# Optimization experiments

Hardware: AMD Instinct MI355X
Metric: run time of the kernel (lower is better)

## Reference

```python
import jax, jax.numpy as jnp
import numpy as np
from jax import lax

ALPHA = 0.95
THETA = 1.0
GAMMA = 12.0
GAIN = 1.0  # gain buffer value used in forward (detached in torch via .item())
KERNELS = (8, 16, 32)
B, T = 256, 16384


@jax.custom_vjp
def surrogate_spike(x):
    # forward: hard threshold at 0
    return (x >= 0).astype(x.dtype)


def _spike_fwd(x):
    return surrogate_spike(x), x


def _spike_bwd(x, g):
    ax = jnp.abs(GAMMA * x)
    grad = (ax < 1.0).astype(x.dtype) * (1.0 - ax) * GAMMA
    return (g * grad,)


surrogate_spike.defvjp(_spike_fwd, _spike_bwd)


def causal_conv(x, w):
    # x: [B,1,T], w: [1,1,k] -> [B,T]; left-pad k-1 (causal), cross-correlation like torch Conv1d
    k = w.shape[-1]
    out = lax.conv_general_dilated(
        x, w, window_strides=(1,), padding=[(k - 1, 0)],
        dimension_numbers=("NCH", "OIH", "NCH"))
    return out[:, 0, :]


def lif_wta(u):
    # u: [B,K,T] -> spikes s_all [B,K,T]
    Bb, K, Tt = u.shape

    def step(v, u_t):  # v,u_t: [B,K]
        v = ALPHA * v + u_t
        m = v - THETA
        s_raw = surrogate_spike(m)
        mask = jax.nn.one_hot(jnp.argmax(m, axis=1), K, dtype=m.dtype)  # top-1 WTA
        s = s_raw * mask
        return v - s * THETA, s

    v0 = jnp.zeros((Bb, K), u.dtype)
    _, s_all = lax.scan(step, v0, jnp.moveaxis(u, 2, 0))  # [T,B,K]
    return jnp.moveaxis(s_all, 0, 2)  # [B,K,T]


def setup_inputs() -> dict:
    key = jax.random.key(0)
    kx, k0, k1, k2, ky = jax.random.split(key, 5)
    x = jax.random.normal(kx, (B, 1, T), dtype=jnp.float32)
    w0 = jax.random.normal(k0, (1, 1, 8), dtype=jnp.float32) / np.sqrt(8.0)
    w1 = jax.random.normal(k1, (1, 1, 16), dtype=jnp.float32) / np.sqrt(16.0)
    w2 = jax.random.normal(k2, (1, 1, 32), dtype=jnp.float32) / np.sqrt(32.0)
    y = jax.random.randint(ky, (B, T), 0, 2, dtype=jnp.int32)
    return {"x": x, "w0": w0, "w1": w1, "w2": w2, "y": y}


def reference(x, w0, w1, w2, y):
    ws = (w0, w1, w2)
    # per-branch causal conv, scaled by 1/sqrt(k), then gain
    u = jnp.stack(
        [causal_conv(x, w) * (1.0 / np.sqrt(float(k))) for w, k in zip(ws, KERNELS)],
        axis=1) * GAIN  # [B,K,T]
    s_all = lif_wta(u)
    return (u, s_all)
```

## Files before the change

kernel.cpp:

```cpp
#include <hip/hip_runtime.h>
#include <math.h>

constexpr int B = 256;
constexpr int T = 16384;
constexpr int K = 3;

constexpr int CHUNK = 256;
constexpr int WARM  = 512;

constexpr int CBT = 128;
constexpr int CWT = 32;


__global__ __launch_bounds__(256, 2) void conv_kernel(
    const float* __restrict__ x,
    const float* __restrict__ w0f,
    const float* __restrict__ w1f,
    const float* __restrict__ w2f,
    float*  __restrict__ u_out,
    float*  __restrict__ w32)
{
    const int blk = blockIdx.x;
    const int bgi = blk >> 7;
    const int t0  = (blk & 127) * CBT;
    const int b0  = bgi * 64;
    const int tid = threadIdx.x;

    __shared__ float sx[64][164];
    for (int k = tid; k < 64 * 40; k += 256) {
        const int r  = k / 40;
        const int c4 = k - r * 40;
        const int g  = t0 - 32 + 4 * c4;
        float4 v = make_float4(0.f, 0.f, 0.f, 0.f);
        if (g >= 0) v = *(const float4*)(x + (size_t)(b0 + r) * T + g);
        *(float4*)&sx[r][4 * c4] = v;
    }
    __syncthreads();

    const int lane    = tid & 63;
    const int w       = tid >> 6;
    const int t_start = t0 + CWT * w;

    double w0d[8], w1d[16], w2d[32];
#pragma unroll
    for (int i = 0; i < 8; ++i)  w0d[i] = (double)w0f[i];
#pragma unroll
    for (int i = 0; i < 16; ++i) w1d[i] = (double)w1f[i];
#pragma unroll
    for (int i = 0; i < 32; ++i) w2d[i] = (double)w2f[i];

    double win[32];
#pragma unroll
    for (int k = 1; k < 32; ++k) win[k] = (double)sx[lane][CWT * w + k];

    const double s8  = 1.0 / sqrt(8.0);
    const double s32 = 1.0 / sqrt(32.0);

    float fr0[16], fr1[16], fr2[16];
    float4 pf;
    float* uf = u_out + (size_t)(b0 + lane) * (3 * T);

#define PPUT(v, D) do {                                                       \
    const float _pv = (v);                                                    \
    if (((D) & 3) == 0) pf.x = _pv;                                           \
    else if (((D) & 3) == 1) pf.y = _pv;                                      \
    else if (((D) & 3) == 2) pf.z = _pv;                                      \
    else {                                                                    \
        pf.w = _pv;                                                           \
        *(float4*)(wq + ((D) >> 2) * 256) = pf;                               \
    }                                                                         \
} while (0)

#pragma unroll
    for (int j = 0; j < CWT; ++j) {
        win[j & 31] = (double)sx[lane][CWT * w + 32 + j];
        double a0 = 0.0, a1 = 0.0, a2 = 0.0;
#pragma unroll
        for (int i = 0; i < 8; ++i)  a0 = fma(w0d[i], win[(j + 25 + i) & 31], a0);
#pragma unroll
        for (int i = 0; i < 16; ++i) a1 = fma(w1d[i], win[(j + 17 + i) & 31], a1);
#pragma unroll
        for (int i = 0; i < 32; ++i) a2 = fma(w2d[i], win[(j + 1 + i) & 31], a2);
        a0 *= s8; a1 *= 0.25; a2 *= s32;

        const int t = t_start + j;
        float* wq = w32 + ((size_t)(t >> 4) * 4 + bgi) * 3072 + lane * 4;
        const int D0 = (j & 15) * 3;
        PPUT((float)(a0 - 0.05), D0);
        PPUT((float)(a1 - 0.05), D0 + 1);
        PPUT((float)(a2 - 0.05), D0 + 2);

        fr0[j & 15] = (float)a0; fr1[j & 15] = (float)a1; fr2[j & 15] = (float)a2;
        if ((j & 15) == 15) {
            float* d = uf + t_start + (j & ~15);
#pragma unroll
            for (int q = 0; q < 4; ++q) {
                *(float4*)(d + 4 * q)         = ((float4*)fr0)[q];
                *(float4*)(d + T + 4 * q)     = ((float4*)fr1)[q];
                *(float4*)(d + 2 * T + 4 * q) = ((float4*)fr2)[q];
            }
        }
    }
#undef PPUT
}

__global__ __launch_bounds__(64, 1) void scan_kernel(
    const float* __restrict__ w32,
    float* __restrict__ s_out)
{
    const int phys = blockIdx.x;
    const int xcd  = phys & 7;
    const int slot = phys >> 3;
    const int c    = 8 * xcd + (slot & 7);
    const int bg   = slot >> 3;
    const int lane = threadIdx.x;

    const int t_emit = c * CHUNK;
    const int t_w    = (t_emit >= WARM) ? (t_emit - WARM) : 0;
    const int warm_g = (t_emit - t_w) >> 4;
    const int n_g    = warm_g + (CHUNK >> 4);
    const int tw16   = t_w >> 4;

    __shared__ float4 lbuf[3 * 768];
    __shared__ float4 sstage[12 * 65];

    double m0 = -1.0, m1 = -1.0, m2 = -1.0;

#define WAITN(N) do {                                                   \
    asm volatile("s_waitcnt vmcnt(" #N ")" ::: "memory");               \
    __builtin_amdgcn_sched_barrier(0);                                  \
} while (0)

#define LOADDMA(s, gg) do {                                                   \
    const float4* _src = (const float4*)(w32 +                                \
        ((size_t)(tw16 + (gg)) * 4 + bg) * 3072) + lane;                      \
    _Pragma("unroll")                                                         \
    for (int _q = 0; _q < 12; ++_q)                                           \
        __builtin_amdgcn_global_load_lds(                                     \
            (const __attribute__((address_space(1))) void*)(const void*)      \
                (_src + (size_t)_q * 64),                                     \
            (__attribute__((address_space(3))) void*)(void*)                  \
                (&lbuf[(s) * 768 + _q * 64]),                                 \
            16, 0, 0);                                                        \
} while (0)

#define STEP(W0, W1, W2, O0, O1, O2) do {                               \
    const double M0 = fma(0.95, m0, (W0));                              \
    const double M1 = fma(0.95, m1, (W1));                              \
    const double M2 = fma(0.95, m2, (W2));                              \
    const bool c01 = (M0 >= M1);                                        \
    const bool c02 = (M0 >= M2);                                        \
    const bool c12 = (M1 >= M2);                                        \
    const bool f0  = (M0 >= 0.0);                                       \
    const bool f1  = (M1 >= 0.0);                                       \
    const bool f2  = (M2 >= 0.0);                                       \
    const bool s0 = c01 & c02 & f0;             \
    const bool s1 = (!c01) & c12 & f1;                                  \
    const bool s2 = (!c02) & (!c12) & f2;                               \
    m0 = s0 ? M0 - 1.0 : M0;                                            \
    m1 = s1 ? M1 - 1.0 : M1;                                            \
    m2 = s2 ? M2 - 1.0 : M2;                                            \
    (O0) = s0 ? 1.0f : 0.0f;                                            \
    (O1) = s1 ? 1.0f : 0.0f;                                            \
    (O2) = s2 ? 1.0f : 0.0f;                                            \
} while (0)

#define GETW(d) ( ((d) & 3) == 0 ? _rf[(d) >> 2].x                      \
                : ((d) & 3) == 1 ? _rf[(d) >> 2].y                      \
                : ((d) & 3) == 2 ? _rf[(d) >> 2].z                      \
                :                  _rf[(d) >> 2].w )

#define BODY(s, pp) do {                                                      \
    if ((pp) < n_g) {                                                         \
        if ((pp) == n_g - 1)            WAITN(24);                            \
        else if ((pp) == n_g - 2)       WAITN(36);                            \
        else if ((pp) >= warm_g + 2)    WAITN(48);                            \
        else if ((pp) == warm_g + 1)    WAITN(36);                            \
        else                            WAITN(24);                            \
        const float4* _lp = lbuf + (s) * 768 + lane;                          \
        float4 _rf[12];                                                       \
        _Pragma("unroll")                                                     \
        for (int _q = 0; _q < 12; ++_q) _rf[_q] = _lp[(size_t)_q * 64];       \
        float sp0[16], sp1[16], sp2[16];                                      \
        _Pragma("unroll")                                                     \
        for (int _j = 0; _j < 16; ++_j) {                                     \
            const int _d0 = 3 * _j;                                           \
            const double _W0 = (double)GETW(_d0);                             \
            const double _W1 = (double)GETW(_d0 + 1);                         \
            const double _W2 = (double)GETW(_d0 + 2);                         \
            STEP(_W0, _W1, _W2, sp0[_j], sp1[_j], sp2[_j]);                   \
        }                                                                     \
        if ((pp) + 3 < n_g) LOADDMA(s, (pp) + 3);                             \
        if ((pp) >= warm_g) {                                                 \
              \
            _Pragma("unroll")                                                 \
            for (int _q = 0; _q < 4; ++_q) {                                  \
                sstage[(0 * 4 + _q) * 65 + lane] = ((float4*)sp0)[_q];        \
                sstage[(1 * 4 + _q) * 65 + lane] = ((float4*)sp1)[_q];        \
                sstage[(2 * 4 + _q) * 65 + lane] = ((float4*)sp2)[_q];        \
            }                                                                 \
            asm volatile("s_waitcnt lgkmcnt(0)" ::: "memory");                \
            __builtin_amdgcn_sched_barrier(0);                                \
              \
              \
            const int _t = t_w + (pp) * 16;                                   \
            _Pragma("unroll")                                                 \
            for (int _k = 0; _k < 3; ++_k) {                                  \
                _Pragma("unroll")                                             \
                for (int _g = 0; _g < 4; ++_g) {                              \
                    const float4 _v =                                         \
                        sstage[(_k * 4 + (lane & 3)) * 65 + _g * 16 + (lane >> 2)]; \
                    float* _dst = s_out                                       \
                        + (size_t)(bg * 64 + _g * 16 + (lane >> 2)) * (3 * T) \
                        + (size_t)_k * T + _t + (lane & 3) * 4;               \
                    *(float4*)_dst = _v;                                      \
                }                                                             \
            }                                                                 \
        }                                                                     \
    }                                                                         \
} while (0)

    LOADDMA(0, 0);
    LOADDMA(1, 1);
    LOADDMA(2, 2);
    for (int p = 0; p < n_g; p += 3) {
        BODY(0, p);
        BODY(1, p + 1);
        BODY(2, p + 2);
    }

#undef BODY
#undef GETW
#undef STEP
#undef LOADDMA
#undef WAITN
}

extern "C" void kernel_launch(void* const* d_in, const int* in_sizes, int n_in,
                              void* d_out, int out_size, void* d_ws, size_t ws_size,
                              hipStream_t stream)
{
    const float* x  = (const float*)d_in[0];
    const float* w0 = (const float*)d_in[1];
    const float* w1 = (const float*)d_in[2];
    const float* w2 = (const float*)d_in[3];

    float* out   = (float*)d_out;
    float* u_out = out;
    float* s_out = out + (size_t)B * K * T;

    float* w32 = (float*)d_ws;

    conv_kernel<<<(B / 64) * (T / CBT), 256, 0, stream>>>(x, w0, w1, w2, u_out, w32);
    scan_kernel<<<B, 64, 0, stream>>>(w32, s_out);
}
```

Before: 217.0 us.

## Split scan chunk across four waves with shared LDS ring and staggered warm-up

The scan kernel moves from one 64-lane wave per block to four waves. Each wave handles a quarter of the 256-step emit chunk and runs its own warm-up window, so the serial dependent chain each wave walks gets shorter. The waves share one 6-slot LDS ring filled by global_load_lds, with each wave issuing a third of each group's loads, and block-wide syncthreads around every group. The cost is duplicated warm-up computation, two barriers per group, and more LDS use.

```diff
diff --git a/kernel.cpp b/kernel.cpp
--- a/kernel.cpp
+++ b/kernel.cpp
@@ -104,7 +104,7 @@
 #undef PPUT
 }
 
-__global__ __launch_bounds__(64, 1) void scan_kernel(
+__global__ __launch_bounds__(256, 1) void scan_kernel(
     const float* __restrict__ w32,
     float* __restrict__ s_out)
 {
@@ -113,16 +113,20 @@
     const int slot = phys >> 3;
     const int c    = 8 * xcd + (slot & 7);
     const int bg   = slot >> 3;
-    const int lane = threadIdx.x;
+    const int tid  = threadIdx.x;
+    const int lane = tid & 63;
+    const int w    = tid >> 6;
 
     const int t_emit = c * CHUNK;
     const int t_w    = (t_emit >= WARM) ? (t_emit - WARM) : 0;
-    const int warm_g = (t_emit - t_w) >> 4;
-    const int n_g    = warm_g + (CHUNK >> 4);
     const int tw16   = t_w >> 4;
-
-    __shared__ float4 lbuf[3 * 768];
-    __shared__ float4 sstage[12 * 65];
+    const int n_g    = (t_emit >> 4) + 16 - tw16;
+    const int es     = n_g - 16 + 4 * w;
+    const int as     = (es >= 32) ? (es - 32) : 0;
+
+    __shared__ float4 ring[6 * 768];
+    __shared__ float4 sstage[4][12 * 65];
+    float4* ss = sstage[w];
 
     double m0 = -1.0, m1 = -1.0, m2 = -1.0;
 
@@ -131,16 +135,16 @@
     __builtin_amdgcn_sched_barrier(0);                                  \
 } while (0)
 
-#define LOADDMA(s, gg) do {                                                   \
+#define ISSUE(sl, gg) do {                                                    \
     const float4* _src = (const float4*)(w32 +                                \
-        ((size_t)(tw16 + (gg)) * 4 + bg) * 3072) + lane;                      \
+        ((size_t)(tw16 + (gg)) * 4 + bg) * 3072) + (size_t)(3 * w) * 64 + lane; \
     _Pragma("unroll")                                                         \
-    for (int _q = 0; _q < 12; ++_q)                                           \
+    for (int _q = 0; _q < 3; ++_q)                                            \
         __builtin_amdgcn_global_load_lds(                                     \
             (const __attribute__((address_space(1))) void*)(const void*)      \
                 (_src + (size_t)_q * 64),                                     \
             (__attribute__((address_space(3))) void*)(void*)                  \
-                (&lbuf[(s) * 768 + _q * 64]),                                 \
+                (&ring[(sl) * 768 + (3 * w + _q) * 64]),                      \
             16, 0, 0);                                                        \
 } while (0)
 
@@ -165,74 +169,75 @@
     (O2) = s2 ? 1.0f : 0.0f;                                            \
 } while (0)
 
-#define GETW(d) ( ((d) & 3) == 0 ? _rf[(d) >> 2].x                      \
-                : ((d) & 3) == 1 ? _rf[(d) >> 2].y                      \
-                : ((d) & 3) == 2 ? _rf[(d) >> 2].z                      \
-                :                  _rf[(d) >> 2].w )
-
-#define BODY(s, pp) do {                                                      \
-    if ((pp) < n_g) {                                                         \
-        if ((pp) == n_g - 1)            WAITN(24);                            \
-        else if ((pp) == n_g - 2)       WAITN(36);                            \
-        else if ((pp) >= warm_g + 2)    WAITN(48);                            \
-        else if ((pp) == warm_g + 1)    WAITN(36);                            \
-        else                            WAITN(24);                            \
-        const float4* _lp = lbuf + (s) * 768 + lane;                          \
-        float4 _rf[12];                                                       \
-        _Pragma("unroll")                                                     \
-        for (int _q = 0; _q < 12; ++_q) _rf[_q] = _lp[(size_t)_q * 64];       \
-        float sp0[16], sp1[16], sp2[16];                                      \
-        _Pragma("unroll")                                                     \
-        for (int _j = 0; _j < 16; ++_j) {                                     \
-            const int _d0 = 3 * _j;                                           \
-            const double _W0 = (double)GETW(_d0);                             \
-            const double _W1 = (double)GETW(_d0 + 1);                         \
-            const double _W2 = (double)GETW(_d0 + 2);                         \
-            STEP(_W0, _W1, _W2, sp0[_j], sp1[_j], sp2[_j]);                   \
-        }                                                                     \
-        if ((pp) + 3 < n_g) LOADDMA(s, (pp) + 3);                             \
-        if ((pp) >= warm_g) {                                                 \
-              \
-            _Pragma("unroll")                                                 \
-            for (int _q = 0; _q < 4; ++_q) {                                  \
-                sstage[(0 * 4 + _q) * 65 + lane] = ((float4*)sp0)[_q];        \
-                sstage[(1 * 4 + _q) * 65 + lane] = ((float4*)sp1)[_q];        \
-                sstage[(2 * 4 + _q) * 65 + lane] = ((float4*)sp2)[_q];        \
-            }                                                                 \
-            asm volatile("s_waitcnt lgkmcnt(0)" ::: "memory");                \
-            __builtin_amdgcn_sched_barrier(0);                                \
-              \
-              \
-            const int _t = t_w + (pp) * 16;                                   \
-            _Pragma("unroll")                                                 \
-            for (int _k = 0; _k < 3; ++_k) {                                  \
-                _Pragma("unroll")                                             \
-                for (int _g = 0; _g < 4; ++_g) {                              \
-                    const float4 _v =                                         \
-                        sstage[(_k * 4 + (lane & 3)) * 65 + _g * 16 + (lane >> 2)]; \
-                    float* _dst = s_out                                       \
-                        + (size_t)(bg * 64 + _g * 16 + (lane >> 2)) * (3 * T) \
-                        + (size_t)_k * T + _t + (lane & 3) * 4;               \
-                    *(float4*)_dst = _v;                                      \
-                }                                                             \
-            }                                                                 \
-        }                                                                     \
-    }                                                                         \
-} while (0)
-
-    LOADDMA(0, 0);
-    LOADDMA(1, 1);
-    LOADDMA(2, 2);
-    for (int p = 0; p < n_g; p += 3) {
-        BODY(0, p);
-        BODY(1, p + 1);
-        BODY(2, p + 2);
+#define GETW(d) ( ((d) & 3) == 0 ? (double)_rf[(d) >> 2].x              \
+                : ((d) & 3) == 1 ? (double)_rf[(d) >> 2].y              \
+                : ((d) & 3) == 2 ? (double)_rf[(d) >> 2].z              \
+                :                  (double)_rf[(d) >> 2].w )
+
+#pragma unroll
+    for (int g = 0; g < 6; ++g) ISSUE(g, g);
+
+    for (int p = 0; p < 48; ++p) {
+        if (p >= n_g) break;
+
+        {
+            const int d = n_g - p;
+            if (d >= 6)      WAITN(15);
+            else if (d == 5) WAITN(12);
+            else if (d == 4) WAITN(9);
+            else if (d == 3) WAITN(6);
+            else if (d == 2) WAITN(3);
+            else             WAITN(0);
+        }
+        __syncthreads();
+
+        const int sl = p % 6;
+        const bool act = (p >= as) && (p < es + 4);
+        float sp0[16], sp1[16], sp2[16];
+        if (act) {
+            const float4* _lp = ring + sl * 768 + lane;
+            float4 _rf[12];
+#pragma unroll
+            for (int _q = 0; _q < 12; ++_q) _rf[_q] = _lp[(size_t)_q * 64];
+#pragma unroll
+            for (int _j = 0; _j < 16; ++_j) {
+                const int _d0 = 3 * _j;
+                STEP(GETW(_d0), GETW(_d0 + 1), GETW(_d0 + 2),
+                     sp0[_j], sp1[_j], sp2[_j]);
+            }
+        }
+        __syncthreads();
+
+        if (p + 6 < n_g) ISSUE(sl, p + 6);
+
+        if (act && p >= es) {
+#pragma unroll
+            for (int _q = 0; _q < 4; ++_q) {
+                ss[(0 * 4 + _q) * 65 + lane] = ((float4*)sp0)[_q];
+                ss[(1 * 4 + _q) * 65 + lane] = ((float4*)sp1)[_q];
+                ss[(2 * 4 + _q) * 65 + lane] = ((float4*)sp2)[_q];
+            }
+            asm volatile("s_waitcnt lgkmcnt(0)" ::: "memory");
+            __builtin_amdgcn_sched_barrier(0);
+            const int _t = (tw16 + p) * 16;
+#pragma unroll
+            for (int _k = 0; _k < 3; ++_k) {
+#pragma unroll
+                for (int _g = 0; _g < 4; ++_g) {
+                    const float4 _v =
+                        ss[(_k * 4 + (lane & 3)) * 65 + _g * 16 + (lane >> 2)];
+                    float* _dst = s_out
+                        + (size_t)(bg * 64 + _g * 16 + (lane >> 2)) * (3 * T)
+                        + (size_t)_k * T + _t + (lane & 3) * 4;
+                    *(float4*)_dst = _v;
+                }
+            }
+        }
     }
 
-#undef BODY
 #undef GETW
 #undef STEP
-#undef LOADDMA
+#undef ISSUE
 #undef WAITN
 }
 
@@ -252,5 +257,5 @@
     float* w32 = (float*)d_ws;
 
     conv_kernel<<<(B / 64) * (T / CBT), 256, 0, stream>>>(x, w0, w1, w2, u_out, w32);
-    scan_kernel<<<B, 64, 0, stream>>>(w32, s_out);
+    scan_kernel<<<B, 256, 0, stream>>>(w32, s_out);
 }
```

Result: slower. 233.1 us (+7.4%).

## Drop the workspace intermediate and have the scan read u directly from the output

Applied to the files above, without the earlier changes.

The conv kernel no longer writes a second interleaved, offset copy of the conv results into the workspace. The scan kernel now streams each lane's own row of u straight from the output buffer with async global-to-LDS loads and subtracts the 0.05 offset itself. This removes a full extra write pass of the u-sized intermediate. In exchange the scan loads become per-row 16-byte strided accesses rather than contiguous tiles. The threshold input is now rounded from the float u rather than from the double value, which could flip rare borderline spikes.

```diff
diff --git a/kernel.cpp b/kernel.cpp
--- a/kernel.cpp
+++ b/kernel.cpp
@@ -17,8 +17,7 @@
     const float* __restrict__ w0f,
     const float* __restrict__ w1f,
     const float* __restrict__ w2f,
-    float*  __restrict__ u_out,
-    float*  __restrict__ w32)
+    float*  __restrict__ u_out)
 {
     const int blk = blockIdx.x;
     const int bgi = blk >> 7;
@@ -57,19 +56,7 @@
     const double s32 = 1.0 / sqrt(32.0);
 
     float fr0[16], fr1[16], fr2[16];
-    float4 pf;
     float* uf = u_out + (size_t)(b0 + lane) * (3 * T);
-
-#define PPUT(v, D) do {                                                       \
-    const float _pv = (v);                                                    \
-    if (((D) & 3) == 0) pf.x = _pv;                                           \
-    else if (((D) & 3) == 1) pf.y = _pv;                                      \
-    else if (((D) & 3) == 2) pf.z = _pv;                                      \
-    else {                                                                    \
-        pf.w = _pv;                                                           \
-        *(float4*)(wq + ((D) >> 2) * 256) = pf;                               \
-    }                                                                         \
-} while (0)
 
 #pragma unroll
     for (int j = 0; j < CWT; ++j) {
@@ -82,13 +69,6 @@
 #pragma unroll
         for (int i = 0; i < 32; ++i) a2 = fma(w2d[i], win[(j + 1 + i) & 31], a2);
         a0 *= s8; a1 *= 0.25; a2 *= s32;
-
-        const int t = t_start + j;
-        float* wq = w32 + ((size_t)(t >> 4) * 4 + bgi) * 3072 + lane * 4;
-        const int D0 = (j & 15) * 3;
-        PPUT((float)(a0 - 0.05), D0);
-        PPUT((float)(a1 - 0.05), D0 + 1);
-        PPUT((float)(a2 - 0.05), D0 + 2);
 
         fr0[j & 15] = (float)a0; fr1[j & 15] = (float)a1; fr2[j & 15] = (float)a2;
         if ((j & 15) == 15) {
@@ -101,11 +81,10 @@
             }
         }
     }
-#undef PPUT
 }
 
 __global__ __launch_bounds__(64, 1) void scan_kernel(
-    const float* __restrict__ w32,
+    const float* __restrict__ u_out,
     float* __restrict__ s_out)
 {
     const int phys = blockIdx.x;
@@ -126,22 +105,25 @@
 
     double m0 = -1.0, m1 = -1.0, m2 = -1.0;
 
+    const float* ub = u_out + (size_t)(bg * 64 + lane) * (3 * T);
+
 #define WAITN(N) do {                                                   \
     asm volatile("s_waitcnt vmcnt(" #N ")" ::: "memory");               \
     __builtin_amdgcn_sched_barrier(0);                                  \
 } while (0)
 
 #define LOADDMA(s, gg) do {                                                   \
-    const float4* _src = (const float4*)(w32 +                                \
-        ((size_t)(tw16 + (gg)) * 4 + bg) * 3072) + lane;                      \
+    const float* _sb = ub + (size_t)(tw16 + (gg)) * 16;                       \
     _Pragma("unroll")                                                         \
-    for (int _q = 0; _q < 12; ++_q)                                           \
-        __builtin_amdgcn_global_load_lds(                                     \
-            (const __attribute__((address_space(1))) void*)(const void*)      \
-                (_src + (size_t)_q * 64),                                     \
-            (__attribute__((address_space(3))) void*)(void*)                  \
-                (&lbuf[(s) * 768 + _q * 64]),                                 \
-            16, 0, 0);                                                        \
+    for (int _k = 0; _k < 3; ++_k)                                            \
+        _Pragma("unroll")                                                     \
+        for (int _tq = 0; _tq < 4; ++_tq)                                     \
+            __builtin_amdgcn_global_load_lds(                                 \
+                (const __attribute__((address_space(1))) void*)(const void*)  \
+                    (_sb + (size_t)_k * T + 4 * _tq),                         \
+                (__attribute__((address_space(3))) void*)(void*)              \
+                    (&lbuf[(s) * 768 + (_k * 4 + _tq) * 64]),                 \
+                16, 0, 0);                                                    \
 } while (0)
 
 #define STEP(W0, W1, W2, O0, O1, O2) do {                               \
@@ -165,16 +147,17 @@
     (O2) = s2 ? 1.0f : 0.0f;                                            \
 } while (0)
 
-#define GETW(d) ( ((d) & 3) == 0 ? _rf[(d) >> 2].x                      \
-                : ((d) & 3) == 1 ? _rf[(d) >> 2].y                      \
-                : ((d) & 3) == 2 ? _rf[(d) >> 2].z                      \
-                :                  _rf[(d) >> 2].w )
+#define GETC(q, cc) ( (cc) == 0 ? _rf[q].x                              \
+                    : (cc) == 1 ? _rf[q].y                              \
+                    : (cc) == 2 ? _rf[q].z : _rf[q].w )
+#define GETWK(k, j) ((double)GETC((k) * 4 + ((j) >> 2), (j) & 3))
 
 #define BODY(s, pp) do {                                                      \
     if ((pp) < n_g) {                                                         \
-        if ((pp) == n_g - 1)            WAITN(24);                            \
-        else if ((pp) == n_g - 2)       WAITN(36);                            \
-        else if ((pp) >= warm_g + 2)    WAITN(48);                            \
+        if ((pp) == n_g - 1)            WAITN(36);                            \
+        else if ((pp) == n_g - 2)       WAITN(48);                            \
+        else if ((pp) >= warm_g + 3)    WAITN(60);                            \
+        else if ((pp) == warm_g + 2)    WAITN(48);                            \
         else if ((pp) == warm_g + 1)    WAITN(36);                            \
         else                            WAITN(24);                            \
         const float4* _lp = lbuf + (s) * 768 + lane;                          \
@@ -184,15 +167,11 @@
         float sp0[16], sp1[16], sp2[16];                                      \
         _Pragma("unroll")                                                     \
         for (int _j = 0; _j < 16; ++_j) {                                     \
-            const int _d0 = 3 * _j;                                           \
-            const double _W0 = (double)GETW(_d0);                             \
-            const double _W1 = (double)GETW(_d0 + 1);                         \
-            const double _W2 = (double)GETW(_d0 + 2);                         \
-            STEP(_W0, _W1, _W2, sp0[_j], sp1[_j], sp2[_j]);                   \
+            STEP(GETWK(0, _j) - 0.05, GETWK(1, _j) - 0.05,                    \
+                 GETWK(2, _j) - 0.05, sp0[_j], sp1[_j], sp2[_j]);             \
         }                                                                     \
         if ((pp) + 3 < n_g) LOADDMA(s, (pp) + 3);                             \
         if ((pp) >= warm_g) {                                                 \
-              \
             _Pragma("unroll")                                                 \
             for (int _q = 0; _q < 4; ++_q) {                                  \
                 sstage[(0 * 4 + _q) * 65 + lane] = ((float4*)sp0)[_q];        \
@@ -201,8 +180,6 @@
             }                                                                 \
             asm volatile("s_waitcnt lgkmcnt(0)" ::: "memory");                \
             __builtin_amdgcn_sched_barrier(0);                                \
-              \
-              \
             const int _t = t_w + (pp) * 16;                                   \
             _Pragma("unroll")                                                 \
             for (int _k = 0; _k < 3; ++_k) {                                  \
@@ -230,7 +207,8 @@
     }
 
 #undef BODY
-#undef GETW
+#undef GETWK
+#undef GETC
 #undef STEP
 #undef LOADDMA
 #undef WAITN
@@ -248,9 +226,8 @@
     float* out   = (float*)d_out;
     float* u_out = out;
     float* s_out = out + (size_t)B * K * T;
-
-    float* w32 = (float*)d_ws;
-
-    conv_kernel<<<(B / 64) * (T / CBT), 256, 0, stream>>>(x, w0, w1, w2, u_out, w32);
-    scan_kernel<<<B, 64, 0, stream>>>(w32, s_out);
+    (void)d_ws; (void)ws_size;
+
+    conv_kernel<<<(B / 64) * (T / CBT), 256, 0, stream>>>(x, w0, w1, w2, u_out);
+    scan_kernel<<<B, 64, 0, stream>>>(u_out, s_out);
 }
```

Measured after the change: 227.3 us. +4.7%, slower.
